# Optimization experiments

Hardware: AMD Instinct MI355X
Metric: run time of the kernel (lower is better)

## Reference

```python
import jax, jax.numpy as jnp
import numpy as np

N_NODES = 50000
N_EDGES = 800000
IN_FEAT = 128
INTER_DIM = 128
OUT_FEAT = 128
EDGE_W_DIM = 3


def setup_inputs() -> dict:
    key = jax.random.key(0)
    ks = jax.random.split(key, 8)
    h = jax.random.normal(ks[0], (N_NODES, IN_FEAT), dtype=jnp.float32)
    edge_src = jax.random.randint(ks[1], (N_EDGES,), 0, N_NODES, dtype=jnp.int32)
    edge_dst = jax.random.randint(ks[2], (N_EDGES,), 0, N_NODES, dtype=jnp.int32)
    edge_w = jax.random.normal(ks[3], (N_EDGES, EDGE_W_DIM), dtype=jnp.float32)
    # xavier-normal-ish init, gain for relu
    gain = float(np.sqrt(2.0))
    W1 = jax.random.normal(ks[4], (INTER_DIM, IN_FEAT + EDGE_W_DIM), dtype=jnp.float32)
    W1 = W1 * (gain * np.sqrt(2.0 / (INTER_DIM + IN_FEAT + EDGE_W_DIM)))
    b1 = jnp.zeros((INTER_DIM,), dtype=jnp.float32)
    W2 = jax.random.normal(ks[5], (OUT_FEAT, IN_FEAT + INTER_DIM), dtype=jnp.float32)
    W2 = W2 * (gain * np.sqrt(2.0 / (OUT_FEAT + IN_FEAT + INTER_DIM)))
    b2 = jnp.zeros((OUT_FEAT,), dtype=jnp.float32)
    return {"h": h, "edge_src": edge_src, "edge_dst": edge_dst, "edge_w": edge_w,
            "W1": W1, "b1": b1, "W2": W2, "b2": b2}


def reference(h, edge_src, edge_dst, edge_w, W1, b1, W2, b2):
    n_nodes = h.shape[0]
    # per-edge message: concat(src node feature, edge weight) -> [E, in_feat+3]
    m = jnp.concatenate([h[edge_src], edge_w], axis=1)
    # linear1 + leaky_relu (torch default negative_slope=0.01)
    tmp = m @ W1.T + b1  # [E, inter_dim]
    tmp = jnp.where(tmp >= 0, tmp, 0.01 * tmp)
    # mean over incoming edges per destination node; zero-in-degree nodes get 0
    sums = jax.ops.segment_sum(tmp, edge_dst, num_segments=n_nodes)
    counts = jax.ops.segment_sum(jnp.ones((tmp.shape[0],), dtype=tmp.dtype),
                                 edge_dst, num_segments=n_nodes)
    h_N = sums / jnp.maximum(counts, 1.0)[:, None]  # [N, inter_dim]
    # tail: concat + linear2 + relu
    h_total = jnp.concatenate([h, h_N], axis=1)  # [N, in_feat+inter_dim]
    return jax.nn.relu(h_total @ W2.T + b2)
```

## Files before the change

### kernel.cpp

```cpp
#include <hip/hip_runtime.h>
#include <hip/hip_bf16.h>

#define N_NODES 50000
#define N_EDGES 800000
#define N_TILES 3125
#define CSR_BLOCKS 782
#define PROJ_BLOCKS 782
#define BUCKET_CAP 64

typedef __attribute__((ext_vector_type(8))) short short8;
typedef __attribute__((ext_vector_type(4))) float f32x4;
typedef __attribute__((ext_vector_type(2))) float fl2;

#define OFF_G     0
#define OFF_CUR   1600000
#define OFF_W1BP  12866384
#define OFF_BP1   12866896
#define OFF_BP2   12875088


__device__ inline unsigned bf16rne(float f) {
    unsigned u = __float_as_uint(f);
    return (u + 0x7fffu + ((u >> 16) & 1u)) >> 16;
}
__device__ inline unsigned pk2(float lo, float hi) {
    return bf16rne(lo) | (bf16rne(hi) << 16);
}
union FragU { unsigned u[4]; short8 s; uint4 v; };

template <bool HI>
__device__ inline fl2 fp8x2_dec_w(unsigned s) {
#if __has_builtin(__builtin_amdgcn_cvt_pk_f32_fp8)
    return __builtin_amdgcn_cvt_pk_f32_fp8((int)s, HI);
#else
    unsigned v = HI ? (s >> 16) : s;
    fl2 r;
    unsigned lo = v & 0xffu, h2 = (v >> 8) & 0xffu;
    unsigned blo = ((lo & 0x80u) << 24) | ((lo & 0x7fu) << 20);
    unsigned bhi = ((h2 & 0x80u) << 24) | ((h2 & 0x7fu) << 20);
    r.x = __uint_as_float(blo) * 0x1p120f;
    r.y = __uint_as_float(bhi) * 0x1p120f;
    return r;
#endif
}
__device__ inline unsigned fp8x4_enc(float a, float b, float c, float d) {
#if __has_builtin(__builtin_amdgcn_cvt_pk_fp8_f32)
    int u = __builtin_amdgcn_cvt_pk_fp8_f32(a, b, 0, false);
    u = __builtin_amdgcn_cvt_pk_fp8_f32(c, d, u, true);
    return (unsigned)u;
#else
    auto enc1 = [](float f) -> unsigned {
        unsigned u = __float_as_uint(f);
        unsigned sg = (u >> 24) & 0x80u;
        float af = fabsf(f);
        if (af < 0x1p-6f) return sg;
        if (af >= 448.f) return sg | 0x7eu;
        unsigned v = __float_as_uint(af);
        unsigned r = v + 0xFFFFFu + ((v >> 20) & 1u);
        unsigned E = r >> 23, m = (r >> 20) & 7u;
        return sg | ((E - 120u) << 3) | m;
    };
    return enc1(a) | (enc1(b) << 8) | (enc1(c) << 16) | (enc1(d) << 24);
#endif
}

__global__ __launch_bounds__(256) void repack_zero_kernel(
        const float* __restrict__ W1, const float* __restrict__ b1,
        const float* __restrict__ W2, float* __restrict__ W1bp,
        uint4* __restrict__ Bpack1, uint4* __restrict__ Bpack2,
        int* __restrict__ cursor) {
    int tid = blockIdx.x * 256 + threadIdx.x;
    if (tid < 2048) {
        int lane = tid & 63, ent = tid >> 6;
        int n = (ent & 7) * 16 + (lane & 15);
        int k0 = (ent >> 3) * 32 + ((lane >> 4) << 3);
        const float* src = W1 + n * 131 + k0;
        FragU f;
        f.u[0] = pk2(src[0], src[1]);
        f.u[1] = pk2(src[2], src[3]);
        f.u[2] = pk2(src[4], src[5]);
        f.u[3] = pk2(src[6], src[7]);
        Bpack1[ent * 64 + lane] = f.v;
    } else if (tid < 6144) {
        int t2 = tid - 2048;
        int lane = t2 & 63, ent = t2 >> 6;
        int n = (ent & 7) * 16 + (lane & 15);
        int k0 = (ent >> 3) * 32 + ((lane >> 4) << 3);
        const float* src = W2 + n * 256 + k0;
        FragU f;
        f.u[0] = pk2(src[0], src[1]);
        f.u[1] = pk2(src[2], src[3]);
        f.u[2] = pk2(src[4], src[5]);
        f.u[3] = pk2(src[6], src[7]);
        Bpack2[ent * 64 + lane] = f.v;
    }
    if (tid < 128) {
        W1bp[tid * 4 + 0] = W1[tid * 131 + 128];
        W1bp[tid * 4 + 1] = W1[tid * 131 + 129];
        W1bp[tid * 4 + 2] = W1[tid * 131 + 130];
        W1bp[tid * 4 + 3] = b1[tid];
    }
    if (tid < N_NODES) cursor[tid] = 0;
}

__global__ __launch_bounds__(256) void fused_bucket_proj(
        const int* __restrict__ esrc, const int* __restrict__ edst,
        const float* __restrict__ ew, int* __restrict__ cursor,
        uint2* __restrict__ bkt,
        const float* __restrict__ h, const uint4* __restrict__ Bpack1,
        unsigned* __restrict__ g8) {
    __shared__ float lds[64][132];
    const int role = blockIdx.x & 1;
    const int gb = blockIdx.x >> 1;

    if (role == 0) {
        const int base = gb * 1024 + threadIdx.x;
        int dst[4], src[4];
        float w0[4], w1[4], w2[4];
        bool ok[4];
        #pragma unroll
        for (int j = 0; j < 4; j++) {
            int e = base + j * 256;
            ok[j] = e < N_EDGES;
            int ce = ok[j] ? e : 0;
            dst[j] = edst[ce];
            src[j] = esrc[ce];
            w0[j] = ew[ce * 3 + 0];
            w1[j] = ew[ce * 3 + 1];
            w2[j] = ew[ce * 3 + 2];
        }
        int pos[4];
        #pragma unroll
        for (int j = 0; j < 4; j++)
            pos[j] = ok[j] ? atomicAdd(&cursor[dst[j]], 1) : BUCKET_CAP;
        #pragma unroll
        for (int j = 0; j < 4; j++) {
            if (ok[j] && pos[j] < BUCKET_CAP) {
                uint2 rec;
                rec.x = (unsigned)src[j] | (bf16rne(w0[j]) << 16);
                rec.y = bf16rne(w1[j]) | (bf16rne(w2[j]) << 16);
                bkt[(dst[j] << 6) + pos[j]] = rec;
            }
        }
        return;
    }

    const int wave = threadIdx.x >> 6;
    const int lane = threadIdx.x & 63;
    const int T = gb * 4 + wave;

    if (T < N_TILES) {
        f32x4 acc[8];
        #pragma unroll
        for (int i = 0; i < 8; i++) acc[i] = (f32x4)(0.f);

        const int row = T * 16 + (lane & 15);
        const float* hrow = h + row * 128 + ((lane >> 4) << 3);

        #pragma unroll
        for (int kt = 0; kt < 4; kt++) {
            float4 x0 = *(const float4*)(hrow + kt * 32);
            float4 x1 = *(const float4*)(hrow + kt * 32 + 4);
            FragU a;
            a.u[0] = pk2(x0.x, x0.y);
            a.u[1] = pk2(x0.z, x0.w);
            a.u[2] = pk2(x1.x, x1.y);
            a.u[3] = pk2(x1.z, x1.w);
            #pragma unroll
            for (int nt = 0; nt < 8; nt++) {
                FragU b;
                b.v = Bpack1[(kt * 8 + nt) * 64 + lane];
                acc[nt] = __builtin_amdgcn_mfma_f32_16x16x32_bf16(a.s, b.s, acc[nt], 0, 0, 0);
            }
        }
        #pragma unroll
        for (int nt = 0; nt < 8; nt++) {
            #pragma unroll
            for (int reg = 0; reg < 4; reg++) {
                int r = ((lane >> 4) << 2) + reg;
                lds[wave * 16 + r][nt * 16 + (lane & 15)] = acc[nt][reg];
            }
        }
    }
    __syncthreads();

    const int t = threadIdx.x;
    const int nodeL = t >> 2, seg = t & 3;
    const int gnode = gb * 64 + nodeL;
    if (gnode < N_NODES) {
        #pragma unroll
        for (int i = 0; i < 2; i++) {
            const float* p = &lds[nodeL][seg * 32 + i * 16];
            uint4 o;
            o.x = fp8x4_enc(p[0],  p[1],  p[2],  p[3]);
            o.y = fp8x4_enc(p[4],  p[5],  p[6],  p[7]);
            o.z = fp8x4_enc(p[8],  p[9],  p[10], p[11]);
            o.w = fp8x4_enc(p[12], p[13], p[14], p[15]);
            ((uint4*)g8)[gnode * 8 + seg * 2 + i] = o;
        }
    }
}

#define AGG_P 4
__global__ __launch_bounds__(256) void fused_agg_final(
        const unsigned* __restrict__ g8u, const uint2* __restrict__ bkt,
        const int* __restrict__ cursor, const float* __restrict__ W1bp,
        const float* __restrict__ h, const uint4* __restrict__ Bpack2,
        const float* __restrict__ b2, float* __restrict__ out) {
    __shared__ float lds[64][132];
    const int wave = threadIdx.x >> 6;
    const int lane = threadIdx.x & 63;
    const int T = blockIdx.x * 4 + wave;

    if (T < N_TILES) {
        const int half = lane >> 5;
        const int c = lane & 31;
        const float4 w0 = ((const float4*)W1bp)[4 * c + 0];
        const float4 w1 = ((const float4*)W1bp)[4 * c + 1];
        const float4 w2 = ((const float4*)W1bp)[4 * c + 2];
        const float4 w3 = ((const float4*)W1bp)[4 * c + 3];
        const fl2 cx0 = {w0.x, w1.x}, cx1 = {w2.x, w3.x};
        const fl2 cy0 = {w0.y, w1.y}, cy1 = {w2.y, w3.y};
        const fl2 cz0 = {w0.z, w1.z}, cz1 = {w2.z, w3.z};
        const fl2 cb0 = {w0.w, w1.w}, cb1 = {w2.w, w3.w};
        const fl2 kP = (fl2)(0.505f);
        const fl2 kA = (fl2)(0.495f);

        for (int n = 0; n < 16; n++) {
            const int v = T * 16 + n;
            const int degT = cursor[v];
            const int deg = (degT < BUCKET_CAP) ? degT : BUCKET_CAP;
            const int beg = v << 6;
            const int end = beg + deg;

            fl2 acc0 = (fl2)(0.f), acc1 = (fl2)(0.f);
            int i = beg;
            for (; i + 2 * AGG_P <= end; i += 2 * AGG_P) {
                uint2 r[AGG_P];
                #pragma unroll
                for (int u = 0; u < AGG_P; u++) r[u] = bkt[i + 2 * u + half];
                unsigned gv[AGG_P];
                #pragma unroll
                for (int u = 0; u < AGG_P; u++) gv[u] = g8u[(r[u].x & 0xffffu) * 32 + c];
                #pragma unroll
                for (int u = 0; u < AGG_P; u++) {
                    fl2 ry = (fl2)(__uint_as_float(r[u].x & 0xffff0000u));
                    fl2 rz = (fl2)(__uint_as_float(r[u].y << 16));
                    fl2 rw = (fl2)(__uint_as_float(r[u].y & 0xffff0000u));
                    fl2 t0 = fp8x2_dec_w<false>(gv[u]) + cb0;
                    t0 = __builtin_elementwise_fma(cx0, ry, t0);
                    t0 = __builtin_elementwise_fma(cy0, rz, t0);
                    t0 = __builtin_elementwise_fma(cz0, rw, t0);
                    acc0 = __builtin_elementwise_fma(kP, t0, acc0);
                    acc0 = __builtin_elementwise_fma(kA, __builtin_elementwise_abs(t0), acc0);
                    fl2 t1 = fp8x2_dec_w<true>(gv[u]) + cb1;
                    t1 = __builtin_elementwise_fma(cx1, ry, t1);
                    t1 = __builtin_elementwise_fma(cy1, rz, t1);
                    t1 = __builtin_elementwise_fma(cz1, rw, t1);
                    acc1 = __builtin_elementwise_fma(kP, t1, acc1);
                    acc1 = __builtin_elementwise_fma(kA, __builtin_elementwise_abs(t1), acc1);
                }
            }
            for (; i + 2 <= end; i += 2) {
                uint2 r = bkt[i + half];
                unsigned gv = g8u[(r.x & 0xffffu) * 32 + c];
                fl2 ry = (fl2)(__uint_as_float(r.x & 0xffff0000u));
                fl2 rz = (fl2)(__uint_as_float(r.y << 16));
                fl2 rw = (fl2)(__uint_as_float(r.y & 0xffff0000u));
                fl2 t0 = fp8x2_dec_w<false>(gv) + cb0;
                t0 = __builtin_elementwise_fma(cx0, ry, t0);
                t0 = __builtin_elementwise_fma(cy0, rz, t0);
                t0 = __builtin_elementwise_fma(cz0, rw, t0);
                acc0 = __builtin_elementwise_fma(kP, t0, acc0);
                acc0 = __builtin_elementwise_fma(kA, __builtin_elementwise_abs(t0), acc0);
                fl2 t1 = fp8x2_dec_w<true>(gv) + cb1;
                t1 = __builtin_elementwise_fma(cx1, ry, t1);
                t1 = __builtin_elementwise_fma(cy1, rz, t1);
                t1 = __builtin_elementwise_fma(cz1, rw, t1);
                acc1 = __builtin_elementwise_fma(kP, t1, acc1);
                acc1 = __builtin_elementwise_fma(kA, __builtin_elementwise_abs(t1), acc1);
            }
            if (i < end) {
                float sc = (half == 0) ? 1.f : 0.f;
                fl2 sP = (fl2)(0.505f * sc), sA = (fl2)(0.495f * sc);
                uint2 r = bkt[i];
                unsigned gv = g8u[(r.x & 0xffffu) * 32 + c];
                fl2 ry = (fl2)(__uint_as_float(r.x & 0xffff0000u));
                fl2 rz = (fl2)(__uint_as_float(r.y << 16));
                fl2 rw = (fl2)(__uint_as_float(r.y & 0xffff0000u));
                fl2 t0 = fp8x2_dec_w<false>(gv) + cb0;
                t0 = __builtin_elementwise_fma(cx0, ry, t0);
                t0 = __builtin_elementwise_fma(cy0, rz, t0);
                t0 = __builtin_elementwise_fma(cz0, rw, t0);
                acc0 = __builtin_elementwise_fma(sP, t0, acc0);
                acc0 = __builtin_elementwise_fma(sA, __builtin_elementwise_abs(t0), acc0);
                fl2 t1 = fp8x2_dec_w<true>(gv) + cb1;
                t1 = __builtin_elementwise_fma(cx1, ry, t1);
                t1 = __builtin_elementwise_fma(cy1, rz, t1);
                t1 = __builtin_elementwise_fma(cz1, rw, t1);
                acc1 = __builtin_elementwise_fma(sP, t1, acc1);
                acc1 = __builtin_elementwise_fma(sA, __builtin_elementwise_abs(t1), acc1);
            }

            acc0.x += __shfl_xor(acc0.x, 32);
            acc0.y += __shfl_xor(acc0.y, 32);
            acc1.x += __shfl_xor(acc1.x, 32);
            acc1.y += __shfl_xor(acc1.y, 32);
            if (half == 0) {
                float inv = 1.0f / (float)((degT > 0) ? degT : 1);
                float4 o;
                o.x = acc0.x * inv;
                o.y = acc0.y * inv;
                o.z = acc1.x * inv;
                o.w = acc1.y * inv;
                *(float4*)&lds[wave * 16 + n][4 * c] = o;
            }
        }
    }
    __syncthreads();

    if (T >= N_TILES) return;

    f32x4 acc[8];
    #pragma unroll
    for (int i = 0; i < 8; i++) acc[i] = (f32x4)(0.f);

    const int row = T * 16 + (lane & 15);
    const int koff = (lane >> 4) << 3;
    const float* hrow = h + row * 128 + koff;
    const float* nrow = &lds[wave * 16 + (lane & 15)][koff];

    #pragma unroll
    for (int kt = 0; kt < 8; kt++) {
        const float* src = (kt < 4) ? (hrow + kt * 32) : (nrow + (kt - 4) * 32);
        float4 x0 = *(const float4*)(src);
        float4 x1 = *(const float4*)(src + 4);
        FragU a;
        a.u[0] = pk2(x0.x, x0.y);
        a.u[1] = pk2(x0.z, x0.w);
        a.u[2] = pk2(x1.x, x1.y);
        a.u[3] = pk2(x1.z, x1.w);
        #pragma unroll
        for (int nt = 0; nt < 8; nt++) {
            FragU b;
            b.v = Bpack2[(kt * 8 + nt) * 64 + lane];
            acc[nt] = __builtin_amdgcn_mfma_f32_16x16x32_bf16(a.s, b.s, acc[nt], 0, 0, 0);
        }
    }
    #pragma unroll
    for (int nt = 0; nt < 8; nt++) {
        int ch = nt * 16 + (lane & 15);
        float bias = b2[ch];
        #pragma unroll
        for (int reg = 0; reg < 4; reg++) {
            int node = T * 16 + ((lane >> 4) << 2) + reg;
            out[node * 128 + ch] = fmaxf(acc[nt][reg] + bias, 0.f);
        }
    }
}

extern "C" void kernel_launch(void* const* d_in, const int* in_sizes, int n_in,
                              void* d_out, int out_size, void* d_ws, size_t ws_size,
                              hipStream_t stream) {
    const float* h    = (const float*)d_in[0];
    const int*   esrc = (const int*)d_in[1];
    const int*   edst = (const int*)d_in[2];
    const float* ew   = (const float*)d_in[3];
    const float* W1   = (const float*)d_in[4];
    const float* b1   = (const float*)d_in[5];
    const float* W2   = (const float*)d_in[6];
    const float* b2   = (const float*)d_in[7];
    float* out = (float*)d_out;
    float* ws  = (float*)d_ws;

    unsigned* g8  = (unsigned*)(ws + OFF_G);
    int* cursor   = (int*)(ws + OFF_CUR);
    float* W1bp   = ws + OFF_W1BP;
    uint4* Bpack1 = (uint4*)(ws + OFF_BP1);
    uint4* Bpack2 = (uint4*)(ws + OFF_BP2);

    uint2* bkt = (uint2*)d_out;

    repack_zero_kernel<<<196, 256, 0, stream>>>(W1, b1, W2, W1bp, Bpack1, Bpack2, cursor);

    fused_bucket_proj<<<CSR_BLOCKS + PROJ_BLOCKS, 256, 0, stream>>>(
        esrc, edst, ew, cursor, bkt, h, Bpack1, g8);

    fused_agg_final<<<(N_TILES + 3) / 4, 256, 0, stream>>>(
        g8, bkt, cursor, W1bp, h, Bpack2, b2, out);
}
```

Before: 200.1 us.

## Assign one 16-node tile per block, splitting aggregation and output columns across waves

The final kernel now launches one block per 16-node tile instead of one tile per wave. Each wave aggregates 4 of the tile's nodes into a shared 16-row LDS buffer. After a barrier, each wave computes 2 of the 8 output column tiles with MFMA. This is meant to spread the irregular per-node gather work across more blocks and shrink LDS per block for better occupancy and load balance. In exchange, every wave reloads the same h rows and A fragments, and there are four times as many blocks to schedule.

```diff
diff --git a/kernel.cpp b/kernel.cpp
--- a/kernel.cpp
+++ b/kernel.cpp
@@ -202,17 +202,17 @@
 }
 
 #define AGG_P 4
-__global__ __launch_bounds__(256) void fused_agg_final(
+__global__ __launch_bounds__(256) void fused_tile_kernel(
         const unsigned* __restrict__ g8u, const uint2* __restrict__ bkt,
         const int* __restrict__ cursor, const float* __restrict__ W1bp,
         const float* __restrict__ h, const uint4* __restrict__ Bpack2,
         const float* __restrict__ b2, float* __restrict__ out) {
-    __shared__ float lds[64][132];
+    __shared__ float lds[16][132];
     const int wave = threadIdx.x >> 6;
     const int lane = threadIdx.x & 63;
-    const int T = blockIdx.x * 4 + wave;
-
-    if (T < N_TILES) {
+    const int T = blockIdx.x;
+
+    {
         const int half = lane >> 5;
         const int c = lane & 31;
         const float4 w0 = ((const float4*)W1bp)[4 * c + 0];
@@ -226,8 +226,10 @@
         const fl2 kP = (fl2)(0.505f);
         const fl2 kA = (fl2)(0.495f);
 
-        for (int n = 0; n < 16; n++) {
-            const int v = T * 16 + n;
+        #pragma unroll
+        for (int n = 0; n < 4; n++) {
+            const int nl = wave * 4 + n;
+            const int v = T * 16 + nl;
             const int degT = cursor[v];
             const int deg = (degT < BUCKET_CAP) ? degT : BUCKET_CAP;
             const int beg = v << 6;
@@ -313,22 +315,20 @@
                 o.y = acc0.y * inv;
                 o.z = acc1.x * inv;
                 o.w = acc1.y * inv;
-                *(float4*)&lds[wave * 16 + n][4 * c] = o;
+                *(float4*)&lds[nl][4 * c] = o;
             }
         }
     }
     __syncthreads();
 
-    if (T >= N_TILES) return;
-
-    f32x4 acc[8];
-    #pragma unroll
-    for (int i = 0; i < 8; i++) acc[i] = (f32x4)(0.f);
-
-    const int row = T * 16 + (lane & 15);
+    f32x4 acc[2];
+    acc[0] = (f32x4)(0.f);
+    acc[1] = (f32x4)(0.f);
+
+    const int aRow = lane & 15;
     const int koff = (lane >> 4) << 3;
-    const float* hrow = h + row * 128 + koff;
-    const float* nrow = &lds[wave * 16 + (lane & 15)][koff];
+    const float* hrow = h + (T * 16 + aRow) * 128 + koff;
+    const float* nrow = &lds[aRow][koff];
 
     #pragma unroll
     for (int kt = 0; kt < 8; kt++) {
@@ -341,20 +341,21 @@
         a.u[2] = pk2(x1.x, x1.y);
         a.u[3] = pk2(x1.z, x1.w);
         #pragma unroll
-        for (int nt = 0; nt < 8; nt++) {
+        for (int q = 0; q < 2; q++) {
+            int nt = wave * 2 + q;
             FragU b;
             b.v = Bpack2[(kt * 8 + nt) * 64 + lane];
-            acc[nt] = __builtin_amdgcn_mfma_f32_16x16x32_bf16(a.s, b.s, acc[nt], 0, 0, 0);
+            acc[q] = __builtin_amdgcn_mfma_f32_16x16x32_bf16(a.s, b.s, acc[q], 0, 0, 0);
         }
     }
     #pragma unroll
-    for (int nt = 0; nt < 8; nt++) {
-        int ch = nt * 16 + (lane & 15);
+    for (int q = 0; q < 2; q++) {
+        int ch = (wave * 2 + q) * 16 + (lane & 15);
         float bias = b2[ch];
         #pragma unroll
         for (int reg = 0; reg < 4; reg++) {
             int node = T * 16 + ((lane >> 4) << 2) + reg;
-            out[node * 128 + ch] = fmaxf(acc[nt][reg] + bias, 0.f);
+            out[node * 128 + ch] = fmaxf(acc[q][reg] + bias, 0.f);
         }
     }
 }
@@ -386,6 +387,6 @@
     fused_bucket_proj<<<CSR_BLOCKS + PROJ_BLOCKS, 256, 0, stream>>>(
         esrc, edst, ew, cursor, bkt, h, Bpack1, g8);
 
-    fused_agg_final<<<(N_TILES + 3) / 4, 256, 0, stream>>>(
+    fused_tile_kernel<<<N_TILES, 256, 0, stream>>>(
         g8, bkt, cursor, W1bp, h, Bpack2, b2, out);
 }
```

Result: no change. 202.5 us (+1.2%).
